# Kernel optimization log

Hardware: AMD Instinct MI355X
Metric: run time of the kernel (lower is better)

The kernel has to match this reference:

```python
import jax, jax.numpy as jnp
import numpy as np

PADDED_NODE_ID = -1
B, N, F = 4096, 128, 64


def setup_inputs() -> dict:
    key = jax.random.key(0)
    k1, k2, k3, k4, k5, k6 = jax.random.split(key, 6)
    src_ids = jax.random.randint(k1, (B, N), 0, 1000, dtype=jnp.int64 if jax.config.jax_enable_x64 else jnp.int32)
    dst_ids = jax.random.randint(k2, (B, N), 0, 1000, dtype=src_ids.dtype)
    w1 = jax.random.normal(k3, (F, 1), dtype=jnp.float32) * 0.1
    b1 = jax.random.normal(k4, (F,), dtype=jnp.float32) * 0.1
    w2 = jax.random.normal(k5, (F, F), dtype=jnp.float32) * 0.1
    b2 = jax.random.normal(k6, (F,), dtype=jnp.float32) * 0.1
    return {"src_neighbour_nodes_ids": src_ids, "dst_neighbour_nodes_ids": dst_ids,
            "w1": w1, "b1": b1, "w2": w2, "b2": b2}


def _pairwise_count(a, b):
    # count[b, i] = #{ j : a[b, i] == b[b, j] }  -- batched histogram via equality
    eq = a[:, :, None] == b[:, None, :]  # [B, N, N] bool
    return eq.sum(axis=-1).astype(jnp.float32)


def _mlp(freq, w1, b1, w2, b2):
    # freq: [B, N, 2] -> Linear(1,F) -> ReLU -> Linear(F,F), then sum over dim 2
    h = freq[..., None] * w1[:, 0] + b1          # [B, N, 2, F]
    h = jax.nn.relu(h)
    out = jnp.einsum('bncf,gf->bncg', h, w2) + b2  # [B, N, 2, F]
    return out.sum(axis=2)                        # [B, N, F]


def reference(src_neighbour_nodes_ids, dst_neighbour_nodes_ids, w1, b1, w2, b2):
    src, dst = src_neighbour_nodes_ids, dst_neighbour_nodes_ids
    src_in_src = _pairwise_count(src, src)
    dst_in_dst = _pairwise_count(dst, dst)
    src_in_dst = _pairwise_count(src, dst)
    dst_in_src = _pairwise_count(dst, src)

    src_pad = (src == PADDED_NODE_ID)[..., None]
    dst_pad = (dst == PADDED_NODE_ID)[..., None]
    source_freq = jnp.where(src_pad, 0.0, jnp.stack([src_in_src, src_in_dst], axis=-1))  # [B,N,2]
    dst_freq = jnp.where(dst_pad, 0.0, jnp.stack([dst_in_dst, dst_in_src], axis=-1))      # [B,N,2]

    src_feat = _mlp(source_freq, w1, b1, w2, b2)
    dst_feat = _mlp(dst_freq, w1, b1, w2, b2)
    return src_feat, dst_feat
```

## Files before the change

### kernel.cpp

```cpp
#include <hip/hip_runtime.h>

#define BATCH 4096
#define NN 128
#define FF 64
#define NC 129
#define HIST 1000
#define PADDED_ID (-1)

__global__ void build_table_kernel(const float* __restrict__ w1,
                                   const float* __restrict__ b1,
                                   const float* __restrict__ w2,
                                   const float* __restrict__ b2,
                                   float* __restrict__ table) {
    int c = blockIdx.x;
    int g = threadIdx.x;
    float cf = (float)c;
    float acc = b2[g];
    #pragma unroll
    for (int f = 0; f < FF; ++f) {
        float h = cf * w1[f] + b1[f];
        h = h > 0.0f ? h : 0.0f;
        acc += h * w2[g * FF + f];
    }
    table[c * FF + g] = acc;
}

__global__ __launch_bounds__(256, 8)
void encode_kernel(const int* __restrict__ src,
                   const int* __restrict__ dst,
                   const float* __restrict__ table,
                   float* __restrict__ out) {
    __shared__ unsigned s_hist[HIST];
    __shared__ unsigned s_cnt[2 * NN];

    const int b   = blockIdx.x;
    const int tid = threadIdx.x;

    const int my = (tid < NN) ? src[b * NN + tid] : dst[b * NN + (tid - NN)];
    const unsigned inc = (tid < NN) ? 1u : 0x10000u;
    const bool valid = (my != PADDED_ID) && ((unsigned)my < HIST);

    #pragma unroll
    for (int i = tid; i < HIST; i += 256) s_hist[i] = 0u;
    __syncthreads();

    if (valid) atomicAdd(&s_hist[my], inc);
    __syncthreads();

    s_cnt[tid] = valid ? s_hist[my] : 0u;
    __syncthreads();

    const int g4 = tid & 15;
    const int n0 = tid >> 4;
    const float4* __restrict__ tab4 = (const float4*)table;
    float4* out_src = (float4*)out + (size_t)b * (NN * FF / 4);
    float4* out_dst = out_src + (size_t)BATCH * (NN * FF / 4);

    #pragma unroll
    for (int n = n0; n < NN; n += 16) {
        {
            const unsigned h = s_cnt[n];
            float4 v0 = tab4[(h & 0xffffu) * (FF / 4) + g4];
            float4 v1 = tab4[(h >> 16)     * (FF / 4) + g4];
            float4 r;
            r.x = v0.x + v1.x; r.y = v0.y + v1.y;
            r.z = v0.z + v1.z; r.w = v0.w + v1.w;
            out_src[n * (FF / 4) + g4] = r;
        }
        {
            const unsigned h = s_cnt[NN + n];
            float4 v0 = tab4[(h & 0xffffu) * (FF / 4) + g4];
            float4 v1 = tab4[(h >> 16)     * (FF / 4) + g4];
            float4 r;
            r.x = v0.x + v1.x; r.y = v0.y + v1.y;
            r.z = v0.z + v1.z; r.w = v0.w + v1.w;
            out_dst[n * (FF / 4) + g4] = r;
        }
    }
}

extern "C" void kernel_launch(void* const* d_in, const int* in_sizes, int n_in,
                              void* d_out, int out_size, void* d_ws, size_t ws_size,
                              hipStream_t stream) {
    const int*   src = (const int*)d_in[0];
    const int*   dst = (const int*)d_in[1];
    const float* w1  = (const float*)d_in[2];
    const float* b1  = (const float*)d_in[3];
    const float* w2  = (const float*)d_in[4];
    const float* b2  = (const float*)d_in[5];
    float* out   = (float*)d_out;
    float* table = (float*)d_ws;

    build_table_kernel<<<NC, FF, 0, stream>>>(w1, b1, w2, b2, table);
    encode_kernel<<<BATCH, 256, 0, stream>>>(src, dst, table, out);
}
```

Baseline: 275.1 us.

## Process two batches per block with prefetch and nontemporal output stores

```diff
diff --git a/kernel.cpp b/kernel.cpp
--- a/kernel.cpp
+++ b/kernel.cpp
@@ -6,6 +6,10 @@
 #define NC 129
 #define HIST 1000
 #define PADDED_ID (-1)
+#define BPB 2
+#define GRID (BATCH / BPB)
+
+typedef float f4 __attribute__((ext_vector_type(4)));
 
 __global__ void build_table_kernel(const float* __restrict__ w1,
                                    const float* __restrict__ b1,
@@ -33,48 +37,53 @@
     __shared__ unsigned s_hist[HIST];
     __shared__ unsigned s_cnt[2 * NN];
 
-    const int b   = blockIdx.x;
     const int tid = threadIdx.x;
+    const unsigned inc = (tid < NN) ? 1u : 0x10000u;
+    const int g4 = tid & 15;
+    const int n0 = tid >> 4;
+    const f4* __restrict__ tab4 = (const f4*)table;
 
-    const int my = (tid < NN) ? src[b * NN + tid] : dst[b * NN + (tid - NN)];
-    const unsigned inc = (tid < NN) ? 1u : 0x10000u;
-    const bool valid = (my != PADDED_ID) && ((unsigned)my < HIST);
+    int b = blockIdx.x * BPB;
+    int my = (tid < NN) ? src[b * NN + tid] : dst[b * NN + (tid - NN)];
 
     #pragma unroll
-    for (int i = tid; i < HIST; i += 256) s_hist[i] = 0u;
-    __syncthreads();
+    for (int k = 0; k < BPB; ++k, ++b) {
+        __syncthreads();
+        #pragma unroll
+        for (int i = tid; i < HIST; i += 256) s_hist[i] = 0u;
+        __syncthreads();
 
-    if (valid) atomicAdd(&s_hist[my], inc);
-    __syncthreads();
+        const bool valid = (my >= 0) && (my < HIST);
+        if (valid) atomicAdd(&s_hist[my], inc);
+        __syncthreads();
 
-    s_cnt[tid] = valid ? s_hist[my] : 0u;
-    __syncthreads();
+        s_cnt[tid] = valid ? s_hist[my] : 0u;
 
-    const int g4 = tid & 15;
-    const int n0 = tid >> 4;
-    const float4* __restrict__ tab4 = (const float4*)table;
-    float4* out_src = (float4*)out + (size_t)b * (NN * FF / 4);
-    float4* out_dst = out_src + (size_t)BATCH * (NN * FF / 4);
+        if (k + 1 < BPB) {
+            const int bn = b + 1;
+            my = (tid < NN) ? src[bn * NN + tid] : dst[bn * NN + (tid - NN)];
+        }
+        __syncthreads();
 
-    #pragma unroll
-    for (int n = n0; n < NN; n += 16) {
-        {
-            const unsigned h = s_cnt[n];
-            float4 v0 = tab4[(h & 0xffffu) * (FF / 4) + g4];
-            float4 v1 = tab4[(h >> 16)     * (FF / 4) + g4];
-            float4 r;
-            r.x = v0.x + v1.x; r.y = v0.y + v1.y;
-            r.z = v0.z + v1.z; r.w = v0.w + v1.w;
-            out_src[n * (FF / 4) + g4] = r;
-        }
-        {
-            const unsigned h = s_cnt[NN + n];
-            float4 v0 = tab4[(h & 0xffffu) * (FF / 4) + g4];
-            float4 v1 = tab4[(h >> 16)     * (FF / 4) + g4];
-            float4 r;
-            r.x = v0.x + v1.x; r.y = v0.y + v1.y;
-            r.z = v0.z + v1.z; r.w = v0.w + v1.w;
-            out_dst[n * (FF / 4) + g4] = r;
+        f4* out_src = (f4*)out + (size_t)b * (NN * FF / 4);
+        f4* out_dst = out_src + (size_t)BATCH * (NN * FF / 4);
+
+        #pragma unroll
+        for (int n = n0; n < NN; n += 16) {
+            {
+                const unsigned h = s_cnt[n];
+                f4 v0 = tab4[(h & 0xffffu) * (FF / 4) + g4];
+                f4 v1 = tab4[(h >> 16)     * (FF / 4) + g4];
+                f4 r = v0 + v1;
+                __builtin_nontemporal_store(r, &out_src[n * (FF / 4) + g4]);
+            }
+            {
+                const unsigned h = s_cnt[NN + n];
+                f4 v0 = tab4[(h & 0xffffu) * (FF / 4) + g4];
+                f4 v1 = tab4[(h >> 16)     * (FF / 4) + g4];
+                f4 r = v0 + v1;
+                __builtin_nontemporal_store(r, &out_dst[n * (FF / 4) + g4]);
+            }
         }
     }
 }
@@ -92,5 +101,5 @@
     float* table = (float*)d_ws;
 
     build_table_kernel<<<NC, FF, 0, stream>>>(w1, b1, w2, b2, table);
-    encode_kernel<<<BATCH, 256, 0, stream>>>(src, dst, table, out);
+    encode_kernel<<<GRID, 256, 0, stream>>>(src, dst, table, out);
 }
```

Measured after the change: 285.7 us. 1.04x slower.
